# Kernel optimization log

Measured on AMD Instinct MI355X. Metric: run time of the kernel, lower is better.

The kernel has to match this reference:

```python
import jax, jax.numpy as jnp
import numpy as np

D_MODEL = 1024
NUM_HEADS = 16
D_K = D_MODEL // NUM_HEADS
B, S = 4, 2048


def setup_inputs() -> dict:
    key = jax.random.key(0)
    ks = jax.random.split(key, 9)
    scale = 1.0 / np.sqrt(D_MODEL)
    x = jax.random.normal(ks[0], (B, S, D_MODEL), dtype=jnp.float32)
    Wq = jax.random.uniform(ks[1], (D_MODEL, D_MODEL), jnp.float32, -scale, scale)
    bq = jax.random.uniform(ks[2], (D_MODEL,), jnp.float32, -scale, scale)
    Wk = jax.random.uniform(ks[3], (D_MODEL, D_MODEL), jnp.float32, -scale, scale)
    bk = jax.random.uniform(ks[4], (D_MODEL,), jnp.float32, -scale, scale)
    Wv = jax.random.uniform(ks[5], (D_MODEL, D_MODEL), jnp.float32, -scale, scale)
    bv = jax.random.uniform(ks[6], (D_MODEL,), jnp.float32, -scale, scale)
    Wo = jax.random.uniform(ks[7], (D_MODEL, D_MODEL), jnp.float32, -scale, scale)
    bo = jax.random.uniform(ks[8], (D_MODEL,), jnp.float32, -scale, scale)
    return {"x": x, "Wq": Wq, "bq": bq, "Wk": Wk, "bk": bk,
            "Wv": Wv, "bv": bv, "Wo": Wo, "bo": bo}


def reference(x, Wq, bq, Wk, bk, Wv, bv, Wo, bo):
    Bsz, Sl, _ = x.shape
    # Linear: x @ W.T + b (torch nn.Linear convention), then split heads -> (B,H,S,d_k)
    def proj(W, b):
        h = jnp.einsum('bsd,ed->bse', x, W) + b
        return h.reshape(Bsz, Sl, NUM_HEADS, D_K).transpose(0, 2, 1, 3)
    q = proj(Wq, bq)
    k = proj(Wk, bk)
    v = proj(Wv, bv)
    scores = jnp.einsum('bhqd,bhkd->bhqk', q, k) / np.sqrt(D_K)
    causal = jnp.tril(jnp.ones((Sl, Sl), dtype=bool))  # True = keep
    scores = jnp.where(causal[None, None], scores, -jnp.inf)
    attn = jax.nn.softmax(scores, axis=-1)
    out = jnp.einsum('bhqk,bhkd->bhqd', attn, v)
    out = out.transpose(0, 2, 1, 3).reshape(Bsz, Sl, D_MODEL)
    return jnp.einsum('bsd,ed->bse', out, Wo) + bo
```

## Files before the change

kernel.cpp:

```cpp
#include <hip/hip_runtime.h>
#include <hip/hip_bf16.h>

typedef __attribute__((ext_vector_type(8))) short short8;
typedef __attribute__((ext_vector_type(4))) short short4v;
typedef __attribute__((ext_vector_type(4))) float floatx4;
typedef unsigned short u16;

#define B_SZ 4
#define NH   16
#define SEQ  2048
#define DM   1024
#define DK   64
#define M_ROWS (B_SZ * SEQ)

__device__ __forceinline__ u16 f2bf(float f) {
  unsigned u = __float_as_uint(f);
  u += 0x7fff + ((u >> 16) & 1);
  return (u16)(u >> 16);
}

__device__ __forceinline__ void async_copy16(const u16* g, const short* lds) {
  __builtin_amdgcn_global_load_lds(
      (const __attribute__((address_space(1))) void*)g,
      (__attribute__((address_space(3))) void*)lds,
      16, 0, 0);
}

__global__ __launch_bounds__(256)
void cvt4_kernel(const float* __restrict__ x,
                 const float* __restrict__ wq, const float* __restrict__ wk,
                 const float* __restrict__ wv,
                 u16* __restrict__ xb, u16* __restrict__ wb)
{
  const int y = blockIdx.y;
  const float* src; u16* dst; int n4;
  if (y == 0)      { src = x;  dst = xb;                 n4 = (M_ROWS * DM) / 4; }
  else if (y == 1) { src = wq; dst = wb;                 n4 = (DM * DM) / 4; }
  else if (y == 2) { src = wk; dst = wb + DM * DM;       n4 = (DM * DM) / 4; }
  else             { src = wv; dst = wb + 2 * DM * DM;   n4 = (DM * DM) / 4; }
  for (int i = blockIdx.x * 256 + threadIdx.x; i < n4; i += gridDim.x * 256) {
    floatx4 v = ((const floatx4*)src)[i];
    short4v s;
#pragma unroll
    for (int e = 0; e < 4; ++e) s[e] = (short)f2bf(v[e]);
    ((short4v*)dst)[i] = s;
  }
}

__global__ __launch_bounds__(256)
void cvt1_kernel(const float* __restrict__ in, u16* __restrict__ out, int n4)
{
  for (int i = blockIdx.x * 256 + threadIdx.x; i < n4; i += gridDim.x * 256) {
    floatx4 v = ((const floatx4*)in)[i];
    short4v s;
#pragma unroll
    for (int e = 0; e < 4; ++e) s[e] = (short)f2bf(v[e]);
    ((short4v*)out)[i] = s;
  }
}

__device__ __forceinline__ void gemm_core_bb(
    const u16* __restrict__ A, const u16* __restrict__ Wb,
    int m0, int n0, floatx4 acc[4][4])
{
  __shared__ short As[128 * 32];
  __shared__ short Bs[128 * 32];

  const int tid  = threadIdx.x;
  const int w    = tid >> 6;
  const int lane = tid & 63;
  const int wm   = w >> 1, wn = w & 1;
  const int quad = lane >> 4, l16 = lane & 15;
  const int r4   = lane >> 2, c4 = lane & 3;

#pragma unroll
  for (int i = 0; i < 4; ++i)
#pragma unroll
    for (int j = 0; j < 4; ++j)
      acc[i][j] = floatx4{0.f, 0.f, 0.f, 0.f};

  for (int kt = 0; kt < (DM >> 5); ++kt) {
    const int kk = kt * 32;
    __syncthreads();
#pragma unroll
    for (int c = 0; c < 2; ++c) {
      const int rowA = w * 32 + c * 16;
      async_copy16(A  + (size_t)(m0 + rowA + r4) * DM + kk + c4 * 8, As + rowA * 32);
      async_copy16(Wb + (size_t)(n0 + rowA + r4) * DM + kk + c4 * 8, Bs + rowA * 32);
    }
    __syncthreads();

    short8 afr[4], bfr[4];
#pragma unroll
    for (int t = 0; t < 4; ++t) {
      afr[t] = *(const short8*)(As + (wm * 64 + t * 16 + l16) * 32 + quad * 8);
      bfr[t] = *(const short8*)(Bs + (wn * 64 + t * 16 + l16) * 32 + quad * 8);
    }
#pragma unroll
    for (int i = 0; i < 4; ++i)
#pragma unroll
      for (int j = 0; j < 4; ++j)
        acc[i][j] = __builtin_amdgcn_mfma_f32_16x16x32_bf16(afr[i], bfr[j], acc[i][j], 0, 0, 0);
  }
}

__global__ __launch_bounds__(256, 2)
void qkv_kernel(const u16* __restrict__ xb, const u16* __restrict__ wb,
                const float* __restrict__ bq, const float* __restrict__ bk,
                const float* __restrict__ bv,
                u16* __restrict__ Qo, u16* __restrict__ Ko, u16* __restrict__ Vto)
{
  const int mat = blockIdx.y >> 3;
  const int m0  = blockIdx.x * 128;
  const int n0  = (blockIdx.y & 7) * 128;
  const u16* W      = wb + (size_t)mat * DM * DM;
  const float* bias = (mat == 0) ? bq : (mat == 1) ? bk : bv;
  u16* dst          = (mat == 0) ? Qo : (mat == 1) ? Ko : Vto;

  floatx4 acc[4][4];
  gemm_core_bb(xb, W, m0, n0, acc);

  const int tid = threadIdx.x;
  const int w = tid >> 6, lane = tid & 63;
  const int wm = w >> 1, wn = w & 1, quad = lane >> 4, l16 = lane & 15;

#pragma unroll
  for (int nt = 0; nt < 4; ++nt) {
    const int n = n0 + wn * 64 + nt * 16 + l16;
    const float bb = bias[n];
    const int h = n >> 6, d = n & 63;
#pragma unroll
    for (int mt = 0; mt < 4; ++mt)
#pragma unroll
      for (int r = 0; r < 4; ++r) {
        const int m = m0 + wm * 64 + mt * 16 + quad * 4 + r;
        const int b = m >> 11, s = m & 2047;
        const float v = acc[mt][nt][r] + bb;
        size_t off;
        if (mat < 2) off = ((size_t)(b * NH + h) * SEQ + s) * DK + d;
        else         off = ((size_t)(b * NH + h) * DK + d) * SEQ + s;
        dst[off] = f2bf(v);
      }
  }
}

#define AT_STR 72
__global__ __launch_bounds__(256, 2)
void attn_kernel(const u16* __restrict__ Q, const u16* __restrict__ Kx,
                 const u16* __restrict__ Vt, u16* __restrict__ O)
{
  __shared__ short Ks[64 * 64];
  __shared__ short Vs[64 * 64];
  __shared__ short Ps[4 * 32 * AT_STR];

  const int bh  = blockIdx.x;
  const int qtb = 15 - (int)blockIdx.y;
  const int q0  = qtb * 128;
  const int tid = threadIdx.x;
  const int w = tid >> 6, lane = tid & 63;
  const int quad = lane >> 4, l16 = lane & 15;
  const int r8 = lane >> 3, c8 = lane & 7;

  const u16* Qh = Q  + (size_t)bh * SEQ * DK;
  const u16* Kh = Kx + (size_t)bh * SEQ * DK;
  const u16* Vh = Vt + (size_t)bh * DK * SEQ;

  short8 qf[2][2];
#pragma unroll
  for (int qp = 0; qp < 2; ++qp) {
    const int qrow = q0 + w * 32 + qp * 16 + l16;
#pragma unroll
    for (int h = 0; h < 2; ++h)
      qf[qp][h] = *(const short8*)(Qh + (size_t)qrow * DK + h * 32 + quad * 8);
  }

  short8 vone;
#pragma unroll
  for (int j = 0; j < 8; ++j) vone[j] = (l16 == 0) ? (short)0x3F80 : (short)0;

  floatx4 o[2][4], ls[2];
#pragma unroll
  for (int qp = 0; qp < 2; ++qp) {
    ls[qp] = floatx4{0.f, 0.f, 0.f, 0.f};
#pragma unroll
    for (int dt = 0; dt < 4; ++dt) o[qp][dt] = floatx4{0.f, 0.f, 0.f, 0.f};
  }

  const float SC2 = 0.18033688011f;
  const int ktmax = 2 * qtb + 2;

  for (int kt = 0; kt < ktmax; ++kt) {
    const int k0 = kt * 64;
    __syncthreads();
#pragma unroll
    for (int c = 0; c < 2; ++c) {
      const int row8 = w * 16 + c * 8;
      const int sw   = (c8 ^ r8) * 8;
      async_copy16(Kh + (size_t)(k0 + row8 + r8) * DK + sw, Ks + row8 * 64);
      async_copy16(Vh + (size_t)(row8 + r8) * SEQ + k0 + sw, Vs + row8 * 64);
    }
    __syncthreads();

    short8 kf[4][2], vf[4][2];
#pragma unroll
    for (int nt = 0; nt < 4; ++nt)
#pragma unroll
      for (int h = 0; h < 2; ++h) {
        kf[nt][h] = *(const short8*)(Ks + (nt * 16 + l16) * 64 + (((h * 4 + quad) ^ (l16 & 7)) * 8));
        vf[nt][h] = *(const short8*)(Vs + (nt * 16 + l16) * 64 + (((h * 4 + quad) ^ (l16 & 7)) * 8));
      }

#pragma unroll
    for (int qp = 0; qp < 2; ++qp) {
      const int frag0 = q0 + w * 32 + qp * 16;
      if (k0 <= frag0 + 15) {
        floatx4 sc[4];
#pragma unroll
        for (int nt = 0; nt < 4; ++nt) {
          floatx4 z = floatx4{0.f, 0.f, 0.f, 0.f};
          z = __builtin_amdgcn_mfma_f32_16x16x32_bf16(qf[qp][0], kf[nt][0], z, 0, 0, 0);
          z = __builtin_amdgcn_mfma_f32_16x16x32_bf16(qf[qp][1], kf[nt][1], z, 0, 0, 0);
          sc[nt] = z;
        }
        const bool diag = (k0 + 63 > frag0);
#pragma unroll
        for (int nt = 0; nt < 4; ++nt)
#pragma unroll
          for (int r = 0; r < 4; ++r) {
            float s = sc[nt][r] * SC2;
            if (diag) {
              const int col = k0 + nt * 16 + l16;
              const int row = frag0 + quad * 4 + r;
              if (col > row) s = -1e30f;
            }
            sc[nt][r] = __builtin_amdgcn_exp2f(s);
          }
        short* Pp = Ps + (w * 32 + qp * 16) * AT_STR;
#pragma unroll
        for (int nt = 0; nt < 4; ++nt)
#pragma unroll
          for (int r = 0; r < 4; ++r)
            Pp[(quad * 4 + r) * AT_STR + nt * 16 + l16] = (short)f2bf(sc[nt][r]);
        short8 pf[2];
#pragma unroll
        for (int h = 0; h < 2; ++h)
          pf[h] = *(const short8*)(Pp + l16 * AT_STR + h * 32 + quad * 8);
#pragma unroll
        for (int dt = 0; dt < 4; ++dt) {
          o[qp][dt] = __builtin_amdgcn_mfma_f32_16x16x32_bf16(pf[0], vf[dt][0], o[qp][dt], 0, 0, 0);
          o[qp][dt] = __builtin_amdgcn_mfma_f32_16x16x32_bf16(pf[1], vf[dt][1], o[qp][dt], 0, 0, 0);
        }
        ls[qp] = __builtin_amdgcn_mfma_f32_16x16x32_bf16(pf[0], vone, ls[qp], 0, 0, 0);
        ls[qp] = __builtin_amdgcn_mfma_f32_16x16x32_bf16(pf[1], vone, ls[qp], 0, 0, 0);
      }
    }
  }

  const int b = bh >> 4, h = bh & 15;
#pragma unroll
  for (int qp = 0; qp < 2; ++qp) {
    const int frag0 = q0 + w * 32 + qp * 16;
#pragma unroll
    for (int r = 0; r < 4; ++r) {
      const float lv  = __shfl(ls[qp][r], lane & 48);
      const float inv = 1.0f / fmaxf(lv, 1e-20f);
      const int row   = frag0 + quad * 4 + r;
      const size_t base = ((size_t)b * SEQ + row) * DM + h * DK;
#pragma unroll
      for (int dt = 0; dt < 4; ++dt)
        O[base + dt * 16 + l16] = f2bf(o[qp][dt][r] * inv);
    }
  }
}

__global__ __launch_bounds__(256, 2)
void oproj_kernel(const u16* __restrict__ A, const u16* __restrict__ Wob,
                  const float* __restrict__ bo, float* __restrict__ out)
{
  const int m0 = blockIdx.x * 128, n0 = blockIdx.y * 128;
  floatx4 acc[4][4];
  gemm_core_bb(A, Wob, m0, n0, acc);

  const int tid = threadIdx.x;
  const int w = tid >> 6, lane = tid & 63;
  const int wm = w >> 1, wn = w & 1, quad = lane >> 4, l16 = lane & 15;

#pragma unroll
  for (int nt = 0; nt < 4; ++nt) {
    const int n = n0 + wn * 64 + nt * 16 + l16;
    const float bb = bo[n];
#pragma unroll
    for (int mt = 0; mt < 4; ++mt)
#pragma unroll
      for (int r = 0; r < 4; ++r) {
        const int m = m0 + wm * 64 + mt * 16 + quad * 4 + r;
        out[(size_t)m * DM + n] = acc[mt][nt][r] + bb;
      }
  }
}

extern "C" void kernel_launch(void* const* d_in, const int* in_sizes, int n_in,
                              void* d_out, int out_size, void* d_ws, size_t ws_size,
                              hipStream_t stream)
{
  const float* x  = (const float*)d_in[0];
  const float* Wq = (const float*)d_in[1];
  const float* bq = (const float*)d_in[2];
  const float* Wk = (const float*)d_in[3];
  const float* bk = (const float*)d_in[4];
  const float* Wv = (const float*)d_in[5];
  const float* bv = (const float*)d_in[6];
  const float* Wo = (const float*)d_in[7];
  const float* bo = (const float*)d_in[8];
  float* out = (float*)d_out;

  u16* qws  = (u16*)d_ws;
  u16* kws  = qws  + (size_t)M_ROWS * DM;
  u16* vtws = kws  + (size_t)M_ROWS * DM;
  u16* ows  = vtws + (size_t)M_ROWS * DM;

  u16* xb = (u16*)d_out;
  u16* wb = xb + (size_t)M_ROWS * DM;
  u16* wo_b = qws;

  cvt4_kernel<<<dim3(1024, 4), 256, 0, stream>>>(x, Wq, Wk, Wv, xb, wb);
  qkv_kernel <<<dim3(64, 24), 256, 0, stream>>>(xb, wb, bq, bk, bv, qws, kws, vtws);
  attn_kernel<<<dim3(64, 16), 256, 0, stream>>>(qws, kws, vtws, ows);
  cvt1_kernel<<<dim3(1024), 256, 0, stream>>>(Wo, wo_b, (DM * DM) / 4);
  oproj_kernel<<<dim3(64, 8), 256, 0, stream>>>(ows, wo_b, bo, out);
}
```

Measured before the change: 280.5 us.

## Replace GEMM core with 256x256 double-buffered swizzled MFMA pipeline for QKV and output projections

Replaces the 128x128, single-buffered, K=32-step GEMM core with a 256x256 tile and 512 threads per block. It double-buffers 64-wide K slices in LDS with an XOR swizzle, overlaps async global-to-LDS loads with MFMA phases, and raises wave priority around the MFMA blocks. The V projection is computed transposed (Wv as A, x as B) so the transposed V stores are contiguous along sequence. Block IDs are remapped for L2 locality. The larger tile cuts global traffic per FLOP and hides load latency, at the cost of fewer blocks (384 and 128), 128KB of LDS per block and many barriers.

```diff
diff --git a/kernel.cpp b/kernel.cpp
--- a/kernel.cpp
+++ b/kernel.cpp
@@ -25,6 +25,9 @@
       (__attribute__((address_space(3))) void*)lds,
       16, 0, 0);
 }
+
+#define BAR() do { __builtin_amdgcn_s_barrier(); asm volatile("" ::: "memory"); } while (0)
+#define WAIT_LGKM0() asm volatile("s_waitcnt lgkmcnt(0)" ::: "memory")
 
 __global__ __launch_bounds__(256)
 void cvt4_kernel(const float* __restrict__ x,
@@ -59,87 +62,214 @@
   }
 }
 
-__device__ __forceinline__ void gemm_core_bb(
-    const u16* __restrict__ A, const u16* __restrict__ Wb,
-    int m0, int n0, floatx4 acc[4][4])
-{
-  __shared__ short As[128 * 32];
-  __shared__ short Bs[128 * 32];
+__device__ __forceinline__ void stage_tile_half(
+    const u16* __restrict__ src,
+    short* dst,
+    int wid, int lane)
+{
+#pragma unroll
+  for (int j = 0; j < 2; ++j) {
+    const int oct = wid + j * 8;
+    const int row = oct * 8 + (lane >> 3);
+    const int cu  = (lane & 7) ^ (lane >> 3);
+    async_copy16(src + (size_t)row * DM + cu * 8, dst + oct * 512);
+  }
+}
+
+__device__ __forceinline__ void gemm256_core(
+    const u16* __restrict__ A, const u16* __restrict__ B,
+    int m0, int n0, floatx4 acc[8][4])
+{
+  __shared__ short smem[65536];
 
   const int tid  = threadIdx.x;
-  const int w    = tid >> 6;
+  const int wid  = tid >> 6;
   const int lane = tid & 63;
-  const int wm   = w >> 1, wn = w & 1;
+  const int wm   = wid >> 2, wn = wid & 3;
   const int quad = lane >> 4, l16 = lane & 15;
-  const int r4   = lane >> 2, c4 = lane & 3;
-
-#pragma unroll
-  for (int i = 0; i < 4; ++i)
-#pragma unroll
-    for (int j = 0; j < 4; ++j)
-      acc[i][j] = floatx4{0.f, 0.f, 0.f, 0.f};
-
-  for (int kt = 0; kt < (DM >> 5); ++kt) {
-    const int kk = kt * 32;
-    __syncthreads();
-#pragma unroll
-    for (int c = 0; c < 2; ++c) {
-      const int rowA = w * 32 + c * 16;
-      async_copy16(A  + (size_t)(m0 + rowA + r4) * DM + kk + c4 * 8, As + rowA * 32);
-      async_copy16(Wb + (size_t)(n0 + rowA + r4) * DM + kk + c4 * 8, Bs + rowA * 32);
+  const int swz  = l16 & 7;
+
+  short* sA_[2] = { smem,         smem + 32768 };
+  short* sB_[2] = { smem + 16384, smem + 49152 };
+
+#pragma unroll
+  for (int mi = 0; mi < 8; ++mi)
+#pragma unroll
+    for (int ni = 0; ni < 4; ++ni)
+      acc[mi][ni] = floatx4{0.f, 0.f, 0.f, 0.f};
+
+  const u16* Abase = A + (size_t)m0 * DM;
+  const u16* Bbase = B + (size_t)n0 * DM;
+
+#pragma unroll
+  for (int t = 0; t < 2; ++t) {
+    const int kof = t * 64;
+    stage_tile_half(Abase + kof,                    sA_[t],        wid, lane);
+    stage_tile_half(Abase + (size_t)128 * DM + kof, sA_[t] + 8192, wid, lane);
+    stage_tile_half(Bbase + kof,                    sB_[t],        wid, lane);
+    stage_tile_half(Bbase + (size_t)128 * DM + kof, sB_[t] + 8192, wid, lane);
+  }
+  asm volatile("s_waitcnt vmcnt(8)" ::: "memory");
+  BAR();
+
+  short8 af[4][2], bf0[2][2], bf1[2][2];
+
+  for (int i = 0; i < 8; ++i) {
+    const bool nl = (i < 7);
+#pragma unroll
+    for (int half = 0; half < 2; ++half) {
+      short* cA = sA_[half];
+      short* cB = sB_[half];
+      const int kof_n = (2 * i + 2 + half) * 64;
+
+#pragma unroll
+      for (int mi = 0; mi < 4; ++mi)
+#pragma unroll
+        for (int kk = 0; kk < 2; ++kk)
+          af[mi][kk] = *(const short8*)(cA + (wm * 128 + mi * 16 + l16) * 64
+                                           + (((kk * 4 + quad) ^ swz) << 3));
+#pragma unroll
+      for (int ni = 0; ni < 2; ++ni)
+#pragma unroll
+        for (int kk = 0; kk < 2; ++kk)
+          bf0[ni][kk] = *(const short8*)(cB + (wn * 64 + ni * 16 + l16) * 64
+                                            + (((kk * 4 + quad) ^ swz) << 3));
+      BAR();
+      WAIT_LGKM0();
+      __builtin_amdgcn_s_setprio(1);
+#pragma unroll
+      for (int mi = 0; mi < 4; ++mi)
+#pragma unroll
+        for (int ni = 0; ni < 2; ++ni)
+#pragma unroll
+          for (int kk = 0; kk < 2; ++kk)
+            acc[mi][ni] = __builtin_amdgcn_mfma_f32_16x16x32_bf16(
+                af[mi][kk], bf0[ni][kk], acc[mi][ni], 0, 0, 0);
+      __builtin_amdgcn_s_setprio(0);
+      BAR();
+
+#pragma unroll
+      for (int ni = 0; ni < 2; ++ni)
+#pragma unroll
+        for (int kk = 0; kk < 2; ++kk)
+          bf1[ni][kk] = *(const short8*)(cB + (wn * 64 + (2 + ni) * 16 + l16) * 64
+                                            + (((kk * 4 + quad) ^ swz) << 3));
+      BAR();
+      WAIT_LGKM0();
+      __builtin_amdgcn_s_setprio(1);
+#pragma unroll
+      for (int mi = 0; mi < 4; ++mi)
+#pragma unroll
+        for (int ni = 0; ni < 2; ++ni)
+#pragma unroll
+          for (int kk = 0; kk < 2; ++kk)
+            acc[mi][2 + ni] = __builtin_amdgcn_mfma_f32_16x16x32_bf16(
+                af[mi][kk], bf1[ni][kk], acc[mi][2 + ni], 0, 0, 0);
+      __builtin_amdgcn_s_setprio(0);
+      BAR();
+
+#pragma unroll
+      for (int mi = 0; mi < 4; ++mi)
+#pragma unroll
+        for (int kk = 0; kk < 2; ++kk)
+          af[mi][kk] = *(const short8*)(cA + (wm * 128 + (4 + mi) * 16 + l16) * 64
+                                           + (((kk * 4 + quad) ^ swz) << 3));
+      if (nl) {
+        stage_tile_half(Bbase + kof_n,                    cB,        wid, lane);
+        stage_tile_half(Bbase + (size_t)128 * DM + kof_n, cB + 8192, wid, lane);
+      }
+      BAR();
+      WAIT_LGKM0();
+      __builtin_amdgcn_s_setprio(1);
+#pragma unroll
+      for (int mi = 0; mi < 4; ++mi)
+#pragma unroll
+        for (int ni = 0; ni < 2; ++ni)
+#pragma unroll
+          for (int kk = 0; kk < 2; ++kk)
+            acc[4 + mi][2 + ni] = __builtin_amdgcn_mfma_f32_16x16x32_bf16(
+                af[mi][kk], bf1[ni][kk], acc[4 + mi][2 + ni], 0, 0, 0);
+      __builtin_amdgcn_s_setprio(0);
+      BAR();
+
+      if (nl) {
+        stage_tile_half(Abase + kof_n,                    cA,        wid, lane);
+        stage_tile_half(Abase + (size_t)128 * DM + kof_n, cA + 8192, wid, lane);
+        asm volatile("s_waitcnt vmcnt(8)" ::: "memory");
+      } else {
+        asm volatile("s_waitcnt vmcnt(0)" ::: "memory");
+      }
+      BAR();
+      __builtin_amdgcn_s_setprio(1);
+#pragma unroll
+      for (int mi = 0; mi < 4; ++mi)
+#pragma unroll
+        for (int ni = 0; ni < 2; ++ni)
+#pragma unroll
+          for (int kk = 0; kk < 2; ++kk)
+            acc[4 + mi][ni] = __builtin_amdgcn_mfma_f32_16x16x32_bf16(
+                af[mi][kk], bf0[ni][kk], acc[4 + mi][ni], 0, 0, 0);
+      __builtin_amdgcn_s_setprio(0);
+      BAR();
     }
-    __syncthreads();
-
-    short8 afr[4], bfr[4];
-#pragma unroll
-    for (int t = 0; t < 4; ++t) {
-      afr[t] = *(const short8*)(As + (wm * 64 + t * 16 + l16) * 32 + quad * 8);
-      bfr[t] = *(const short8*)(Bs + (wn * 64 + t * 16 + l16) * 32 + quad * 8);
+  }
+}
+
+__global__ __launch_bounds__(512, 2)
+void qkv256_kernel(const u16* __restrict__ xb, const u16* __restrict__ wb,
+                   const float* __restrict__ bq, const float* __restrict__ bk,
+                   const float* __restrict__ bv,
+                   u16* __restrict__ Qo, u16* __restrict__ Ko, u16* __restrict__ Vto)
+{
+  const int bx = blockIdx.x;
+  const int wg = (bx & 7) * 48 + (bx >> 3);
+  const int mat = wg >> 7;
+  const int r   = wg & 127;
+
+  int m0, n0;
+  const u16 *A, *Bm;
+  if (mat < 2) { m0 = (r >> 2) * 256; n0 = (r & 3) * 256; A = xb; Bm = wb + (size_t)mat * DM * DM; }
+  else         { m0 = (r & 3) * 256;  n0 = (r >> 2) * 256; A = wb + (size_t)2 * DM * DM; Bm = xb; }
+
+  floatx4 acc[8][4];
+  gemm256_core(A, Bm, m0, n0, acc);
+
+  const int tid = threadIdx.x;
+  const int wid = tid >> 6, lane = tid & 63;
+  const int wm = wid >> 2, wn = wid & 3;
+  const int quad = lane >> 4, l16 = lane & 15;
+
+  if (mat < 2) {
+    u16* dst = (mat == 0) ? Qo : Ko;
+    const float* bias = (mat == 0) ? bq : bk;
+#pragma unroll
+    for (int ni = 0; ni < 4; ++ni) {
+      const int n = n0 + wn * 64 + ni * 16 + l16;
+      const float bb = bias[n];
+      const int h = n >> 6, d = n & 63;
+#pragma unroll
+      for (int mi = 0; mi < 8; ++mi)
+#pragma unroll
+        for (int rr = 0; rr < 4; ++rr) {
+          const int m = m0 + wm * 128 + mi * 16 + quad * 4 + rr;
+          const int b = m >> 11, s = m & 2047;
+          dst[((size_t)(b * NH + h) * SEQ + s) * DK + d] = f2bf(acc[mi][ni][rr] + bb);
+        }
     }
-#pragma unroll
-    for (int i = 0; i < 4; ++i)
-#pragma unroll
-      for (int j = 0; j < 4; ++j)
-        acc[i][j] = __builtin_amdgcn_mfma_f32_16x16x32_bf16(afr[i], bfr[j], acc[i][j], 0, 0, 0);
-  }
-}
-
-__global__ __launch_bounds__(256, 2)
-void qkv_kernel(const u16* __restrict__ xb, const u16* __restrict__ wb,
-                const float* __restrict__ bq, const float* __restrict__ bk,
-                const float* __restrict__ bv,
-                u16* __restrict__ Qo, u16* __restrict__ Ko, u16* __restrict__ Vto)
-{
-  const int mat = blockIdx.y >> 3;
-  const int m0  = blockIdx.x * 128;
-  const int n0  = (blockIdx.y & 7) * 128;
-  const u16* W      = wb + (size_t)mat * DM * DM;
-  const float* bias = (mat == 0) ? bq : (mat == 1) ? bk : bv;
-  u16* dst          = (mat == 0) ? Qo : (mat == 1) ? Ko : Vto;
-
-  floatx4 acc[4][4];
-  gemm_core_bb(xb, W, m0, n0, acc);
-
-  const int tid = threadIdx.x;
-  const int w = tid >> 6, lane = tid & 63;
-  const int wm = w >> 1, wn = w & 1, quad = lane >> 4, l16 = lane & 15;
-
-#pragma unroll
-  for (int nt = 0; nt < 4; ++nt) {
-    const int n = n0 + wn * 64 + nt * 16 + l16;
-    const float bb = bias[n];
-    const int h = n >> 6, d = n & 63;
-#pragma unroll
-    for (int mt = 0; mt < 4; ++mt)
-#pragma unroll
-      for (int r = 0; r < 4; ++r) {
-        const int m = m0 + wm * 64 + mt * 16 + quad * 4 + r;
-        const int b = m >> 11, s = m & 2047;
-        const float v = acc[mt][nt][r] + bb;
-        size_t off;
-        if (mat < 2) off = ((size_t)(b * NH + h) * SEQ + s) * DK + d;
-        else         off = ((size_t)(b * NH + h) * DK + d) * SEQ + s;
-        dst[off] = f2bf(v);
+  } else {
+#pragma unroll
+    for (int mi = 0; mi < 8; ++mi)
+#pragma unroll
+      for (int rr = 0; rr < 4; ++rr) {
+        const int m = m0 + wm * 128 + mi * 16 + quad * 4 + rr;
+        const float bb = bv[m];
+        const int h = m >> 6, d = m & 63;
+#pragma unroll
+        for (int ni = 0; ni < 4; ++ni) {
+          const int n = n0 + wn * 64 + ni * 16 + l16;
+          const int b = n >> 11, s = n & 2047;
+          Vto[((size_t)(b * NH + h) * DK + d) * SEQ + s] = f2bf(acc[mi][ni][rr] + bb);
+        }
       }
   }
 }
@@ -273,28 +403,32 @@
   }
 }
 
-__global__ __launch_bounds__(256, 2)
-void oproj_kernel(const u16* __restrict__ A, const u16* __restrict__ Wob,
-                  const float* __restrict__ bo, float* __restrict__ out)
-{
-  const int m0 = blockIdx.x * 128, n0 = blockIdx.y * 128;
-  floatx4 acc[4][4];
-  gemm_core_bb(A, Wob, m0, n0, acc);
+__global__ __launch_bounds__(512, 2)
+void oproj256_kernel(const u16* __restrict__ A, const u16* __restrict__ Wob,
+                     const float* __restrict__ bo, float* __restrict__ out)
+{
+  const int bx = blockIdx.x;
+  const int wg = (bx & 7) * 16 + (bx >> 3);
+  const int m0 = (wg >> 2) * 256, n0 = (wg & 3) * 256;
+
+  floatx4 acc[8][4];
+  gemm256_core(A, Wob, m0, n0, acc);
 
   const int tid = threadIdx.x;
-  const int w = tid >> 6, lane = tid & 63;
-  const int wm = w >> 1, wn = w & 1, quad = lane >> 4, l16 = lane & 15;
-
-#pragma unroll
-  for (int nt = 0; nt < 4; ++nt) {
-    const int n = n0 + wn * 64 + nt * 16 + l16;
+  const int wid = tid >> 6, lane = tid & 63;
+  const int wm = wid >> 2, wn = wid & 3;
+  const int quad = lane >> 4, l16 = lane & 15;
+
+#pragma unroll
+  for (int ni = 0; ni < 4; ++ni) {
+    const int n = n0 + wn * 64 + ni * 16 + l16;
     const float bb = bo[n];
 #pragma unroll
-    for (int mt = 0; mt < 4; ++mt)
-#pragma unroll
-      for (int r = 0; r < 4; ++r) {
-        const int m = m0 + wm * 64 + mt * 16 + quad * 4 + r;
-        out[(size_t)m * DM + n] = acc[mt][nt][r] + bb;
+    for (int mi = 0; mi < 8; ++mi)
+#pragma unroll
+      for (int rr = 0; rr < 4; ++rr) {
+        const int m = m0 + wm * 128 + mi * 16 + quad * 4 + rr;
+        out[(size_t)m * DM + n] = acc[mi][ni][rr] + bb;
       }
   }
 }
@@ -323,9 +457,9 @@
   u16* wb = xb + (size_t)M_ROWS * DM;
   u16* wo_b = qws;
 
-  cvt4_kernel<<<dim3(1024, 4), 256, 0, stream>>>(x, Wq, Wk, Wv, xb, wb);
-  qkv_kernel <<<dim3(64, 24), 256, 0, stream>>>(xb, wb, bq, bk, bv, qws, kws, vtws);
-  attn_kernel<<<dim3(64, 16), 256, 0, stream>>>(qws, kws, vtws, ows);
-  cvt1_kernel<<<dim3(1024), 256, 0, stream>>>(Wo, wo_b, (DM * DM) / 4);
-  oproj_kernel<<<dim3(64, 8), 256, 0, stream>>>(ows, wo_b, bo, out);
-}
+  cvt4_kernel  <<<dim3(1024, 4), 256, 0, stream>>>(x, Wq, Wk, Wv, xb, wb);
+  qkv256_kernel<<<dim3(384), 512, 0, stream>>>(xb, wb, bq, bk, bv, qws, kws, vtws);
+  attn_kernel  <<<dim3(64, 16), 256, 0, stream>>>(qws, kws, vtws, ows);
+  cvt1_kernel  <<<dim3(1024), 256, 0, stream>>>(Wo, wo_b, (DM * DM) / 4);
+  oproj256_kernel<<<dim3(128), 512, 0, stream>>>(ows, wo_b, bo, out);
+}
```

Result: faster. 269.0 us (-4.1%).
